# Performance work log

Measured on AMD Instinct MI355X. Metric: run time of the kernel, lower is better.

The kernel has to match this reference:

```python
import jax, jax.numpy as jnp
import numpy as np

D = 512
O = 64

def setup_inputs() -> dict:
    key = jax.random.key(0)
    k1, k2, k3, k4 = jax.random.split(key, 4)
    B, N, F, V = 4, 1024, 16, 64
    x = jax.random.normal(k1, (B, N, D), dtype=jnp.float32)
    idx = jax.random.randint(k2, (B, F), 0, V)
    feature_bias_table = jax.random.normal(k3, (V, D), dtype=jnp.float32)
    out_projection_table = jax.random.normal(k4, (V, D * O), dtype=jnp.float32) * (1.0 / np.sqrt(D))
    return {"x": x, "idx": idx, "feature_bias_table": feature_bias_table,
            "out_projection_table": out_projection_table}

def reference(x, idx, feature_bias_table, out_projection_table):
    # x: [B,N,D], idx: [B,F]
    w = out_projection_table[idx].reshape(*idx.shape, D, O)   # [B,F,D,O]
    b = feature_bias_table[idx]                               # [B,F,D]
    xb = x[:, :, None, :] + b[:, None, :, :]                  # [B,N,F,D]
    out = jnp.einsum('bnfd,bfdo->bnfo', xb, w)                # [B,N,F,O]
    return out
```

## Files before the change

kernel.cpp:

```cpp
#include <hip/hip_runtime.h>
#include <hip/hip_bf16.h>
#include <stdint.h>


typedef __bf16 bf16_t;
typedef __bf16 bf16x8 __attribute__((ext_vector_type(8)));
typedef float floatx4 __attribute__((ext_vector_type(4)));

__device__ __forceinline__ void async_ld16(const bf16_t* g, bf16_t* l) {
    __builtin_amdgcn_global_load_lds(
        (const __attribute__((address_space(1))) void*)g,
        (__attribute__((address_space(3))) void*)l,
        16, 0, 0);
}

__global__ __launch_bounds__(256) void prep_kernel(
    const float* __restrict__ w,
    const float* __restrict__ bias,
    const float* __restrict__ x,
    bf16_t* __restrict__ wt,
    float* __restrict__ cv,
    bf16_t* __restrict__ xb)
{
    const int t = threadIdx.x;
    if (blockIdx.x >= 512) {
        const int base = (blockIdx.x - 512) * 2048 + t * 8;
        const float4 f0 = *(const float4*)(x + base);
        const float4 f1 = *(const float4*)(x + base + 4);
        bf16x8 o;
        o[0] = (bf16_t)f0.x; o[1] = (bf16_t)f0.y;
        o[2] = (bf16_t)f0.z; o[3] = (bf16_t)f0.w;
        o[4] = (bf16_t)f1.x; o[5] = (bf16_t)f1.y;
        o[6] = (bf16_t)f1.z; o[7] = (bf16_t)f1.w;
        *(bf16x8*)(xb + base) = o;
        return;
    }

    const int v = blockIdx.x >> 3;
    const int c = blockIdx.x & 7;
    __shared__ float tile[64][68];
    __shared__ float bch[64];
    __shared__ float red[4][64];

    const int r = t >> 2, cs = (t & 3) * 16;
    const float* src = w + (size_t)v * 32768 + (size_t)(c * 64 + r) * 64 + cs;
    *(float4*)&tile[r][cs]      = *(const float4*)(src);
    *(float4*)&tile[r][cs + 4]  = *(const float4*)(src + 4);
    *(float4*)&tile[r][cs + 8]  = *(const float4*)(src + 8);
    *(float4*)&tile[r][cs + 12] = *(const float4*)(src + 12);
    if (t < 64) bch[t] = bias[v * 512 + c * 64 + t];
    __syncthreads();

    const int o = t >> 2, ds = (t & 3) * 16;
    bf16x8 t0, t1;
#pragma unroll
    for (int j = 0; j < 8; ++j) t0[j] = (bf16_t)tile[ds + j][o];
#pragma unroll
    for (int j = 0; j < 8; ++j) t1[j] = (bf16_t)tile[ds + 8 + j][o];
    bf16_t* dst = wt + ((size_t)v * 64 + o) * 512 + c * 64 + ds;
    *(bf16x8*)&dst[0] = t0;
    *(bf16x8*)&dst[8] = t1;

    const int dq = t >> 6, oc = t & 63;
    float csum = 0.f;
#pragma unroll
    for (int j = 0; j < 16; ++j) {
        const int dl = dq * 16 + j;
        csum += bch[dl] * tile[dl][oc];
    }
    red[dq][oc] = csum;
    __syncthreads();
    if (t < 64) atomicAdd(&cv[v * 64 + t],
                          red[0][t] + red[1][t] + red[2][t] + red[3][t]);
}

__global__ __launch_bounds__(256, 2) void gemm_kernel(
    const bf16_t* __restrict__ xb,
    const bf16_t* __restrict__ wt,
    const float*  __restrict__ cv,
    const int*    __restrict__ idx,
    float* __restrict__ out)
{
    const int bid = blockIdx.x;
    const int f  = bid >> 5;
    const int b  = (bid >> 3) & 3;
    const int mt = bid & 7;
    const int v  = idx[b * 16 + f];

    const int tid  = threadIdx.x;
    const int lane = tid & 63;
    const int wave = tid >> 6;
    const int wm = wave >> 1;
    const int wn = wave & 1;
    const int l15 = lane & 15;
    const int l4  = lane >> 4;

    const bf16_t* Ag = xb + (size_t)(b * 1024 + mt * 128) * 512;
    const bf16_t* Bg = wt + (size_t)v * 64 * 512;

    __shared__ __align__(16) bf16_t As[2][128 * 64];

    floatx4 acc[4][2] = {};

    int a_row[4], a_col[4];
#pragma unroll
    for (int j = 0; j < 4; ++j) {
        const int s = tid + 256 * j;
        a_row[j] = s >> 3;
        a_col[j] = ((s & 7) ^ (a_row[j] & 7)) * 8;
    }

    const bf16_t* bp[2];
#pragma unroll
    for (int ni = 0; ni < 2; ++ni)
        bp[ni] = Bg + (size_t)(wn * 32 + ni * 16 + l15) * 512 + l4 * 8;

#pragma unroll
    for (int j = 0; j < 4; ++j)
        async_ld16(Ag + a_row[j] * 512 + a_col[j], &As[0][(tid + 256 * j) * 8]);
    bf16x8 breg[2][2][2];
#pragma unroll
    for (int ni = 0; ni < 2; ++ni)
#pragma unroll
        for (int ks = 0; ks < 2; ++ks)
            breg[0][ni][ks] = *(const bf16x8*)(bp[ni] + ks * 32);

    for (int kk = 0; kk < 8; ++kk) {
        const int buf = kk & 1;
        __syncthreads();
        if (kk < 7) {
            const int k0 = (kk + 1) * 64;
#pragma unroll
            for (int j = 0; j < 4; ++j)
                async_ld16(Ag + a_row[j] * 512 + k0 + a_col[j],
                           &As[buf ^ 1][(tid + 256 * j) * 8]);
#pragma unroll
            for (int ni = 0; ni < 2; ++ni)
#pragma unroll
                for (int ks = 0; ks < 2; ++ks)
                    breg[buf ^ 1][ni][ks] =
                        *(const bf16x8*)(bp[ni] + k0 + ks * 32);
        }
        bf16x8 a[4][2];
#pragma unroll
        for (int mi = 0; mi < 4; ++mi) {
            const int row = wm * 64 + mi * 16 + l15;
#pragma unroll
            for (int ks = 0; ks < 2; ++ks)
                a[mi][ks] = *(const bf16x8*)
                    &As[buf][row * 64 + (((ks * 4 + l4) ^ (row & 7)) * 8)];
        }
#pragma unroll
        for (int mi = 0; mi < 4; ++mi)
#pragma unroll
            for (int ni = 0; ni < 2; ++ni) {
                acc[mi][ni] = __builtin_amdgcn_mfma_f32_16x16x32_bf16(
                    a[mi][0], breg[buf][ni][0], acc[mi][ni], 0, 0, 0);
                acc[mi][ni] = __builtin_amdgcn_mfma_f32_16x16x32_bf16(
                    a[mi][1], breg[buf][ni][1], acc[mi][ni], 0, 0, 0);
            }
    }

    const int colbase = wn * 32 + l15;
    const float c0 = cv[v * 64 + colbase];
    const float c1 = cv[v * 64 + colbase + 16];
    float* outp = out + (size_t)(b * 1024 + mt * 128 + wm * 64 + l4 * 4) * 1024
                      + f * 64;
#pragma unroll
    for (int mi = 0; mi < 4; ++mi) {
#pragma unroll
        for (int r = 0; r < 4; ++r) {
            float* row = outp + (size_t)(mi * 16 + r) * 1024;
            row[colbase]      = acc[mi][0][r] + c0;
            row[colbase + 16] = acc[mi][1][r] + c1;
        }
    }
}

__global__ __launch_bounds__(256) void naive_kernel(
    const float* __restrict__ x, const float* __restrict__ w,
    const float* __restrict__ bias, const int* __restrict__ idx,
    float* __restrict__ out)
{
    const int b = blockIdx.x >> 10;
    const int n = blockIdx.x & 1023;
    __shared__ float xr[512];
    for (int d = threadIdx.x; d < 512; d += 256)
        xr[d] = x[(size_t)(b * 1024 + n) * 512 + d];
    __syncthreads();
    for (int p = threadIdx.x; p < 1024; p += 256) {
        const int f = p >> 6, o = p & 63;
        const int v = idx[b * 16 + f];
        const float* wp = w + (size_t)v * 32768 + o;
        const float* bp = bias + v * 512;
        float s = 0.f;
        for (int d = 0; d < 512; ++d)
            s += (xr[d] + bp[d]) * wp[(size_t)d * 64];
        out[(size_t)(b * 1024 + n) * 1024 + p] = s;
    }
}

extern "C" void kernel_launch(void* const* d_in, const int* in_sizes, int n_in,
                              void* d_out, int out_size, void* d_ws, size_t ws_size,
                              hipStream_t stream) {
    const float* x    = (const float*)d_in[0];
    const int*   idx  = (const int*)d_in[1];
    const float* bias = (const float*)d_in[2];
    const float* w    = (const float*)d_in[3];
    float* out = (float*)d_out;

    const size_t cv_bytes = 64 * 64 * sizeof(float);
    const size_t wt_bytes = (size_t)64 * 64 * 512 * 2;
    const size_t xb_bytes = (size_t)4096 * 512 * 2;
    if (ws_size >= cv_bytes + wt_bytes + xb_bytes) {
        float*  cv = (float*)d_ws;
        bf16_t* wt = (bf16_t*)((char*)d_ws + cv_bytes);
        bf16_t* xb = (bf16_t*)((char*)d_ws + cv_bytes + wt_bytes);
        hipMemsetAsync(cv, 0, cv_bytes, stream);
        prep_kernel<<<1536, 256, 0, stream>>>(w, bias, x, wt, cv, xb);
        gemm_kernel<<<512, 256, 0, stream>>>(xb, wt, cv, idx, out);
    } else {
        naive_kernel<<<4096, 256, 0, stream>>>(x, w, bias, idx, out);
    }
}
```

Measured before the change: 91.24 us.

## Fuse x bf16 conversion into GEMM loads and drop memset via partial bias sums

Result: faster. 89.07 us (-2.4%).

```diff
diff --git a/kernel.cpp b/kernel.cpp
--- a/kernel.cpp
+++ b/kernel.cpp
@@ -7,37 +7,15 @@
 typedef __bf16 bf16x8 __attribute__((ext_vector_type(8)));
 typedef float floatx4 __attribute__((ext_vector_type(4)));
 
-__device__ __forceinline__ void async_ld16(const bf16_t* g, bf16_t* l) {
-    __builtin_amdgcn_global_load_lds(
-        (const __attribute__((address_space(1))) void*)g,
-        (__attribute__((address_space(3))) void*)l,
-        16, 0, 0);
-}
-
 __global__ __launch_bounds__(256) void prep_kernel(
     const float* __restrict__ w,
     const float* __restrict__ bias,
-    const float* __restrict__ x,
     bf16_t* __restrict__ wt,
-    float* __restrict__ cv,
-    bf16_t* __restrict__ xb)
+    float* __restrict__ cvp)
 {
-    const int t = threadIdx.x;
-    if (blockIdx.x >= 512) {
-        const int base = (blockIdx.x - 512) * 2048 + t * 8;
-        const float4 f0 = *(const float4*)(x + base);
-        const float4 f1 = *(const float4*)(x + base + 4);
-        bf16x8 o;
-        o[0] = (bf16_t)f0.x; o[1] = (bf16_t)f0.y;
-        o[2] = (bf16_t)f0.z; o[3] = (bf16_t)f0.w;
-        o[4] = (bf16_t)f1.x; o[5] = (bf16_t)f1.y;
-        o[6] = (bf16_t)f1.z; o[7] = (bf16_t)f1.w;
-        *(bf16x8*)(xb + base) = o;
-        return;
-    }
-
     const int v = blockIdx.x >> 3;
     const int c = blockIdx.x & 7;
+    const int t = threadIdx.x;
     __shared__ float tile[64][68];
     __shared__ float bch[64];
     __shared__ float red[4][64];
@@ -70,14 +48,15 @@
     }
     red[dq][oc] = csum;
     __syncthreads();
-    if (t < 64) atomicAdd(&cv[v * 64 + t],
-                          red[0][t] + red[1][t] + red[2][t] + red[3][t]);
+    if (t < 64)
+        cvp[c * 4096 + v * 64 + t] =
+            red[0][t] + red[1][t] + red[2][t] + red[3][t];
 }
 
 __global__ __launch_bounds__(256, 2) void gemm_kernel(
-    const bf16_t* __restrict__ xb,
+    const float*  __restrict__ x,
     const bf16_t* __restrict__ wt,
-    const float*  __restrict__ cv,
+    const float*  __restrict__ cvp,
     const int*    __restrict__ idx,
     float* __restrict__ out)
 {
@@ -95,19 +74,20 @@
     const int l15 = lane & 15;
     const int l4  = lane >> 4;
 
-    const bf16_t* Ag = xb + (size_t)(b * 1024 + mt * 128) * 512;
+    const float*  Ag = x  + (size_t)(b * 1024 + mt * 128) * 512;
     const bf16_t* Bg = wt + (size_t)v * 64 * 512;
 
     __shared__ __align__(16) bf16_t As[2][128 * 64];
 
     floatx4 acc[4][2] = {};
 
-    int a_row[4], a_col[4];
+    int a_row[4], a_k8[4], a_slot[4];
 #pragma unroll
     for (int j = 0; j < 4; ++j) {
         const int s = tid + 256 * j;
-        a_row[j] = s >> 3;
-        a_col[j] = ((s & 7) ^ (a_row[j] & 7)) * 8;
+        a_row[j]  = s >> 3;
+        a_k8[j]   = s & 7;
+        a_slot[j] = a_k8[j] ^ (a_row[j] & 7);
     }
 
     const bf16_t* bp[2];
@@ -115,25 +95,45 @@
     for (int ni = 0; ni < 2; ++ni)
         bp[ni] = Bg + (size_t)(wn * 32 + ni * 16 + l15) * 512 + l4 * 8;
 
-#pragma unroll
-    for (int j = 0; j < 4; ++j)
-        async_ld16(Ag + a_row[j] * 512 + a_col[j], &As[0][(tid + 256 * j) * 8]);
+    float4 r0[4], r1[4];
     bf16x8 breg[2][2][2];
+
+#define LOAD_A(K0)                                                        \
+    {                                                                     \
+        _Pragma("unroll")                                                 \
+        for (int j = 0; j < 4; ++j) {                                     \
+            const float* p = Ag + a_row[j] * 512 + (K0) + a_k8[j] * 8;    \
+            r0[j] = *(const float4*)p;                                    \
+            r1[j] = *(const float4*)(p + 4);                              \
+        }                                                                 \
+    }
+#define WRITE_A(BUF)                                                      \
+    {                                                                     \
+        _Pragma("unroll")                                                 \
+        for (int j = 0; j < 4; ++j) {                                     \
+            bf16x8 ov;                                                    \
+            ov[0] = (bf16_t)r0[j].x; ov[1] = (bf16_t)r0[j].y;             \
+            ov[2] = (bf16_t)r0[j].z; ov[3] = (bf16_t)r0[j].w;             \
+            ov[4] = (bf16_t)r1[j].x; ov[5] = (bf16_t)r1[j].y;             \
+            ov[6] = (bf16_t)r1[j].z; ov[7] = (bf16_t)r1[j].w;             \
+            *(bf16x8*)&As[BUF][a_row[j] * 64 + a_slot[j] * 8] = ov;       \
+        }                                                                 \
+    }
+
+    LOAD_A(0);
 #pragma unroll
     for (int ni = 0; ni < 2; ++ni)
 #pragma unroll
         for (int ks = 0; ks < 2; ++ks)
             breg[0][ni][ks] = *(const bf16x8*)(bp[ni] + ks * 32);
+    WRITE_A(0);
+    __syncthreads();
 
     for (int kk = 0; kk < 8; ++kk) {
         const int buf = kk & 1;
-        __syncthreads();
         if (kk < 7) {
             const int k0 = (kk + 1) * 64;
-#pragma unroll
-            for (int j = 0; j < 4; ++j)
-                async_ld16(Ag + a_row[j] * 512 + k0 + a_col[j],
-                           &As[buf ^ 1][(tid + 256 * j) * 8]);
+            LOAD_A(k0);
 #pragma unroll
             for (int ni = 0; ni < 2; ++ni)
 #pragma unroll
@@ -159,11 +159,21 @@
                 acc[mi][ni] = __builtin_amdgcn_mfma_f32_16x16x32_bf16(
                     a[mi][1], breg[buf][ni][1], acc[mi][ni], 0, 0, 0);
             }
-    }
+        if (kk < 7) {
+            WRITE_A(buf ^ 1);
+            __syncthreads();
+        }
+    }
+#undef LOAD_A
+#undef WRITE_A
 
     const int colbase = wn * 32 + l15;
-    const float c0 = cv[v * 64 + colbase];
-    const float c1 = cv[v * 64 + colbase + 16];
+    float c0 = 0.f, c1 = 0.f;
+#pragma unroll
+    for (int p = 0; p < 8; ++p) {
+        c0 += cvp[p * 4096 + v * 64 + colbase];
+        c1 += cvp[p * 4096 + v * 64 + colbase + 16];
+    }
     float* outp = out + (size_t)(b * 1024 + mt * 128 + wm * 64 + l4 * 4) * 1024
                       + f * 64;
 #pragma unroll
@@ -209,16 +219,13 @@
     const float* w    = (const float*)d_in[3];
     float* out = (float*)d_out;
 
-    const size_t cv_bytes = 64 * 64 * sizeof(float);
-    const size_t wt_bytes = (size_t)64 * 64 * 512 * 2;
-    const size_t xb_bytes = (size_t)4096 * 512 * 2;
-    if (ws_size >= cv_bytes + wt_bytes + xb_bytes) {
-        float*  cv = (float*)d_ws;
-        bf16_t* wt = (bf16_t*)((char*)d_ws + cv_bytes);
-        bf16_t* xb = (bf16_t*)((char*)d_ws + cv_bytes + wt_bytes);
-        hipMemsetAsync(cv, 0, cv_bytes, stream);
-        prep_kernel<<<1536, 256, 0, stream>>>(w, bias, x, wt, cv, xb);
-        gemm_kernel<<<512, 256, 0, stream>>>(xb, wt, cv, idx, out);
+    const size_t cvp_bytes = (size_t)8 * 64 * 64 * sizeof(float);
+    const size_t wt_bytes  = (size_t)64 * 64 * 512 * 2;
+    if (ws_size >= cvp_bytes + wt_bytes) {
+        float*  cvp = (float*)d_ws;
+        bf16_t* wt  = (bf16_t*)((char*)d_ws + cvp_bytes);
+        prep_kernel<<<512, 256, 0, stream>>>(w, bias, wt, cvp);
+        gemm_kernel<<<512, 256, 0, stream>>>(x, wt, cvp, idx, out);
     } else {
         naive_kernel<<<4096, 256, 0, stream>>>(x, w, bias, idx, out);
     }
```
